# Optimization experiments

Measured on AMD Instinct MI355X. Metric: run time of the kernel, lower is better.

The kernel has to match this reference:

```python
import jax, jax.numpy as jnp
import numpy as np

N, E, H, O = 50000, 640000, 128, 2
N_LAYERS = 3


def setup_inputs() -> dict:
    key = jax.random.key(0)
    ks = jax.random.split(key, 20)
    s = 0.05
    inp = {
        "x": jax.random.normal(ks[0], (N, H), dtype=jnp.float32),
        "edge_index": jax.random.randint(ks[1], (2, E), 0, N, dtype=jnp.int64),
        "edge_type": jax.random.randint(ks[2], (E,), 0, 2, dtype=jnp.int64),
        # msg_sf MLP: Linear(2H->H), ReLU, Linear(H->H)
        "w1_sf": jax.random.normal(ks[3], (2 * H, H), jnp.float32) * s,
        "b1_sf": jnp.zeros((H,), jnp.float32),
        "w2_sf": jax.random.normal(ks[4], (H, H), jnp.float32) * s,
        "b2_sf": jnp.zeros((H,), jnp.float32),
        # msg_fd MLP
        "w1_fd": jax.random.normal(ks[5], (2 * H, H), jnp.float32) * s,
        "b1_fd": jnp.zeros((H,), jnp.float32),
        "w2_fd": jax.random.normal(ks[6], (H, H), jnp.float32) * s,
        "b2_fd": jnp.zeros((H,), jnp.float32),
        # GRUCell gru_h (PyTorch layout: [3H, in] / [3H, H], gate order r,z,n)
        "gru_w_ih": jax.random.normal(ks[7], (3 * H, H), jnp.float32) * s,
        "gru_w_hh": jax.random.normal(ks[8], (3 * H, H), jnp.float32) * s,
        "gru_b_ih": jnp.zeros((3 * H,), jnp.float32),
        "gru_b_hh": jnp.zeros((3 * H,), jnp.float32),
        # readout: Linear(H->H), ReLU, Linear(H->O)
        "wr1": jax.random.normal(ks[9], (H, H), jnp.float32) * s,
        "br1": jnp.zeros((H,), jnp.float32),
        "wr2": jax.random.normal(ks[10], (H, O), jnp.float32) * s,
        "br2": jnp.zeros((O,), jnp.float32),
    }
    return inp


def _mlp(ef, w1, b1, w2, b2):
    return jax.nn.relu(ef @ w1 + b1) @ w2 + b2


def _gru_cell(m, h, w_ih, w_hh, b_ih, b_hh):
    gi = m @ w_ih.T + b_ih  # [N, 3H]
    gh = h @ w_hh.T + b_hh  # [N, 3H]
    r = jax.nn.sigmoid(gi[:, :H] + gh[:, :H])
    z = jax.nn.sigmoid(gi[:, H:2 * H] + gh[:, H:2 * H])
    n = jnp.tanh(gi[:, 2 * H:] + r * gh[:, 2 * H:])
    return (1.0 - z) * n + z * h


def reference(x, edge_index, edge_type,
              w1_sf, b1_sf, w2_sf, b2_sf,
              w1_fd, b1_fd, w2_fd, b2_fd,
              gru_w_ih, gru_w_hh, gru_b_ih, gru_b_hh,
              wr1, br1, wr2, br2):
    src, tgt = edge_index[0], edge_index[1]
    is_sf = (edge_type == 0)[:, None]  # [E, 1]
    h = x
    for _ in range(N_LAYERS):
        # gather source/target node states and concatenate -> [E, 2H]
        ef = jnp.concatenate([h[src], h[tgt]], axis=-1)
        # per-edge message from the edge-type-specific MLP
        m = jnp.where(is_sf,
                      _mlp(ef, w1_sf, b1_sf, w2_sf, b2_sf),
                      _mlp(ef, w1_fd, b1_fd, w2_fd, b2_fd))
        # scatter-add into target nodes
        messages = jax.ops.segment_sum(m, tgt, num_segments=h.shape[0])
        # GRU node update (original's messages.mean(dim=1) is shape-invalid
        # for GRUCell; the runnable interpretation feeds messages directly)
        h = _gru_cell(messages, h, gru_w_ih, gru_w_hh, gru_b_ih, gru_b_hh)
    out = jax.nn.relu(h @ wr1 + br1) @ wr2 + br2
    return jax.nn.softmax(out, axis=1)
```

## Files before the change

### kernel.cpp

```cpp
#include <hip/hip_runtime.h>
#include <hip/hip_bf16.h>


#define NN 50000
#define EE 640000
#define HH 128
#define NBINS (2 * NN)
#define NBLKS 384

typedef __attribute__((ext_vector_type(8))) short short8;
typedef __attribute__((ext_vector_type(4))) float f32x4;

__device__ __forceinline__ unsigned short f2b(float f) {
  __hip_bfloat16 b = __float2bfloat16(f);
  return *reinterpret_cast<unsigned short*>(&b);
}
__device__ __forceinline__ float b2f_lo(unsigned int u) {
  union { unsigned int u; float f; } a; a.u = u << 16; return a.f;
}
__device__ __forceinline__ float b2f_hi(unsigned int u) {
  union { unsigned int u; float f; } a; a.u = u & 0xFFFF0000u; return a.f;
}

__device__ __forceinline__ void gload_lds16(const void* g, void* l) {
  __builtin_amdgcn_global_load_lds((const __attribute__((address_space(1))) void*)g,
                                   (__attribute__((address_space(3))) void*)l, 16, 0, 0);
}

__global__ __launch_bounds__(256) void k_init(const float* __restrict__ x, float* __restrict__ h,
                                              unsigned short* __restrict__ hbf) {
  int i = blockIdx.x * 256 + threadIdx.x;
  float v = x[i];
  h[i] = v;
  hbf[i] = f2b(v);
}

__global__ __launch_bounds__(256) void k_pack(
    const float* __restrict__ w1s, const float* __restrict__ w2s,
    const float* __restrict__ w1f, const float* __restrict__ w2f,
    const float* __restrict__ gwih, const float* __restrict__ gwhh,
    const float* __restrict__ gbih, const float* __restrict__ gbhh,
    unsigned short* __restrict__ pw1s, unsigned short* __restrict__ pw2s,
    unsigned short* __restrict__ pw1f, unsigned short* __restrict__ pw2f,
    unsigned short* __restrict__ pgru, float* __restrict__ bgr) {
  int i = blockIdx.x * 256 + threadIdx.x;
  if (i < 65536) {
    int ty = i >> 15, idx = i & 32767;
    int j = idx & 7, l = (idx >> 3) & 63, kn = idx >> 9;
    int ks = kn & 7, nt = kn >> 3;
    int k = ks * 32 + (l >> 4) * 8 + j, c = nt * 16 + (l & 15);
    const float* w = ty ? w1f : w1s;
    (ty ? pw1f : pw1s)[idx] = f2b(w[k * 128 + c]);
  } else if (i < 98304) {
    int i2 = i - 65536;
    int ty = i2 >> 14, idx = i2 & 16383;
    int j = idx & 7, l = (idx >> 3) & 63, kn = idx >> 9;
    int ks = kn & 3, nt = kn >> 2;
    int k = ks * 32 + (l >> 4) * 8 + j, c = nt * 16 + (l & 15);
    const float* w = ty ? w2f : w2s;
    (ty ? pw2f : pw2s)[idx] = f2b(w[k * 128 + c]);
  } else if (i < 98304 + 131072) {
    int idx = i - 98304;
    int j = idx & 7, l = (idx >> 3) & 63, kc = idx >> 9;
    int ks = kc & 7, ct = kc >> 3;
    int k = ks * 32 + (l >> 4) * 8 + j, c = ct * 16 + (l & 15);
    float v;
    if (c < 256)      v = (k < 128) ? gwih[c * 128 + k] : gwhh[c * 128 + (k - 128)];
    else if (c < 384) v = (k < 128) ? gwih[c * 128 + k] : 0.f;
    else              v = (k >= 128) ? gwhh[(c - 128) * 128 + (k - 128)] : 0.f;
    pgru[idx] = f2b(v);
  } else if (i < 98304 + 131072 + 512) {
    int j = i - (98304 + 131072);
    float v;
    if (j < 256)      v = gbih[j] + gbhh[j];
    else if (j < 384) v = gbih[j];
    else              v = gbhh[j - 128];
    bgr[j] = v;
  }
}

__global__ __launch_bounds__(256) void k_hist(const int* __restrict__ ei, const int* __restrict__ et,
                                              int* __restrict__ hist) {
  int e = blockIdx.x * 256 + threadIdx.x;
  int g = ei[EE + e];
  int ty = et[e];
  atomicAdd(&hist[ty * NN + g], 1);
}

__global__ __launch_bounds__(1024) void k_scan1(const int* __restrict__ hist, int* __restrict__ base,
                                                int* __restrict__ bsum) {
  __shared__ int sh[1024];
  int t = threadIdx.x;
  int i = blockIdx.x * 1024 + t;
  int v = (i < NBINS) ? hist[i] : 0;
  sh[t] = v;
  __syncthreads();
  for (int o = 1; o < 1024; o <<= 1) {
    int xv = (t >= o) ? sh[t - o] : 0;
    __syncthreads();
    sh[t] += xv;
    __syncthreads();
  }
  if (i < NBINS) base[i] = sh[t] - v;
  if (t == 1023) bsum[blockIdx.x] = sh[t];
}

__global__ __launch_bounds__(128) void k_scan2(int* __restrict__ bsum) {
  __shared__ int sh[128];
  int t = threadIdx.x;
  int v = (t < 98) ? bsum[t] : 0;
  sh[t] = v;
  __syncthreads();
  for (int o = 1; o < 128; o <<= 1) {
    int xv = (t >= o) ? sh[t - o] : 0;
    __syncthreads();
    sh[t] += xv;
    __syncthreads();
  }
  if (t < 98) bsum[t] = sh[t] - v;
}

__global__ __launch_bounds__(1024) void k_scan3(const int* __restrict__ bsum, int* __restrict__ base,
                                                int* __restrict__ cnt) {
  int i = blockIdx.x * 1024 + threadIdx.x;
  if (i < NBINS) {
    int b = base[i] + bsum[blockIdx.x];
    base[i] = b;
    if (i == NN) cnt[0] = b;
  }
}

__global__ __launch_bounds__(256) void k_scatter(const int* __restrict__ ei, const int* __restrict__ et,
                                                 int* __restrict__ woff, int* __restrict__ ssrc,
                                                 int* __restrict__ stgt) {
  int e = blockIdx.x * 256 + threadIdx.x;
  int s = ei[e], g = ei[EE + e], ty = et[e];
  int pos = atomicAdd(&woff[ty * NN + g], 1);
  ssrc[pos] = s;
  stgt[pos] = g;
}

__global__ __launch_bounds__(256, 2) void k_edge(
    const unsigned short* __restrict__ hbf,
    const int* __restrict__ ssrc, const int* __restrict__ stgt,
    const unsigned short* __restrict__ pw1s, const unsigned short* __restrict__ pw2s,
    const unsigned short* __restrict__ pw1f, const unsigned short* __restrict__ pw2f,
    const float* __restrict__ b1s, const float* __restrict__ b2s,
    const float* __restrict__ b1f, const float* __restrict__ b2f,
    float* __restrict__ msg, const int* __restrict__ cnt) {
  __shared__ char efA[16384];
  __shared__ char efB[16384];
  __shared__ char mC[17408];
  __shared__ int idxbuf[2][2][64];
  const int tid = threadIdx.x, l = tid & 63, w = tid >> 6;
  const int c0 = cnt[0];
  const int type = (blockIdx.x >= NBLKS) ? 1 : 0;
  const int bsub = type ? (blockIdx.x - NBLKS) : blockIdx.x;
  const int lo = type ? c0 : 0;
  const int hi = type ? EE : c0;
  const int ntile = (hi - lo + 63) >> 6;
  if (bsub >= ntile) return;
  const int nblk = 1 + (ntile - 1 - bsub) / NBLKS;
  const unsigned short* pw1 = type ? pw1f : pw1s;
  const unsigned short* pw2 = type ? pw2f : pw2s;
  const float* b1 = type ? b1f : b1s;
  const float* b2 = type ? b2f : b2s;

  short8 wb1[2][8];
#pragma unroll
  for (int q = 0; q < 2; q++) {
    int nt = 2 * w + q;
#pragma unroll
    for (int ks = 0; ks < 8; ks++)
      wb1[q][ks] = *(const short8*)(pw1 + ((nt * 8 + ks) * 64 + l) * 8);
  }
  float b1v[2], b2v[2];
  b1v[0] = b1[(2 * w) * 16 + (l & 15)];
  b1v[1] = b1[(2 * w + 1) * 16 + (l & 15)];
  b2v[0] = b2[(2 * w) * 16 + (l & 15)];
  b2v[1] = b2[(2 * w + 1) * 16 + (l & 15)];

  auto issue_gathers = [&](int slot) {
#pragma unroll
    for (int i = 0; i < 4; i++) {
      int r = w * 16 + i * 4 + (l >> 4);
      int j = (l & 15) ^ (r & 7);
      int nodeS = idxbuf[slot][0][r];
      gload_lds16(hbf + (size_t)nodeS * HH + j * 8, efA + w * 4096 + i * 1024);
      int nodeT = idxbuf[slot][1][r];
      if (nodeT < 0) nodeT = 0;
      gload_lds16(hbf + (size_t)nodeT * HH + j * 8, efB + w * 4096 + i * 1024);
    }
  };

  {
    int p0 = lo + bsub * 64 + (tid & 63);
    if (tid < 64) {
      int v = (p0 < hi) ? ssrc[p0] : 0;
      if (v < 0) v = 0;
      idxbuf[0][0][tid] = v;
    } else if (tid < 128) {
      int v = (p0 < hi) ? stgt[p0] : -1;
      idxbuf[0][1][tid & 63] = v;
    }
  }
  int ridx = (tid < 64) ? 0 : -1;
  {
    int p1 = lo + (bsub + NBLKS) * 64 + (tid & 63);
    if (tid < 128 && p1 < hi) ridx = (tid < 64) ? ssrc[p1] : stgt[p1];
  }
  asm volatile("s_waitcnt lgkmcnt(0)" ::: "memory");
  __builtin_amdgcn_s_barrier();
  issue_gathers(0);

  f32x4 zero4 = {0.f, 0.f, 0.f, 0.f};
  for (int k = 0; k < nblk; k++) {
    const int cur = k & 1, nxt = cur ^ 1;
    asm volatile("s_waitcnt vmcnt(0)" ::: "memory");
    __builtin_amdgcn_sched_barrier(0);
    __builtin_amdgcn_s_barrier();

    f32x4 acc[4][2];
#pragma unroll
    for (int mt = 0; mt < 4; mt++)
#pragma unroll
      for (int q = 0; q < 2; q++) acc[mt][q] = zero4;
    __builtin_amdgcn_s_setprio(1);
#pragma unroll
    for (int ks = 0; ks < 8; ks++) {
      const char* ef = (ks < 4) ? efA : efB;
      int ko = (ks & 3) * 64;
      short8 a[4];
#pragma unroll
      for (int mt = 0; mt < 4; mt++) {
        int row = mt * 16 + (l & 15);
        a[mt] = *(const short8*)(ef + row * 256 + ((ko + (l >> 4) * 16) ^ ((row & 7) << 4)));
      }
#pragma unroll
      for (int mt = 0; mt < 4; mt++)
#pragma unroll
        for (int q = 0; q < 2; q++)
          acc[mt][q] = __builtin_amdgcn_mfma_f32_16x16x32_bf16(a[mt], wb1[q][ks], acc[mt][q], 0, 0, 0);
    }
    __builtin_amdgcn_s_setprio(0);
    if (tid < 128) {
      int v = ridx;
      if (tid < 64 && v < 0) v = 0;
      idxbuf[nxt][tid >= 64 ? 1 : 0][tid & 63] = v;
    }
    {
      int p2 = lo + (bsub + (k + 2) * NBLKS) * 64 + (tid & 63);
      ridx = (tid < 64) ? 0 : -1;
      if (tid < 128 && p2 < hi) ridx = (tid < 64) ? ssrc[p2] : stgt[p2];
    }
#pragma unroll
    for (int mt = 0; mt < 4; mt++)
#pragma unroll
      for (int q = 0; q < 2; q++) {
        int col = (2 * w + q) * 16 + (l & 15);
#pragma unroll
        for (int r = 0; r < 4; r++) {
          int row = mt * 16 + (l >> 4) * 4 + r;
          float v = acc[mt][q][r] + b1v[q];
          v = v > 0.f ? v : 0.f;
          *(unsigned short*)(mC + row * 256 + ((col * 2) ^ ((row & 7) << 4))) = f2b(v);
        }
      }
    asm volatile("s_waitcnt lgkmcnt(0)" ::: "memory");
    __builtin_amdgcn_s_barrier();

    short8 wb2[2][4];
#pragma unroll
    for (int q = 0; q < 2; q++)
#pragma unroll
      for (int ks = 0; ks < 4; ks++)
        wb2[q][ks] = *(const short8*)(pw2 + (((2 * w + q) * 4 + ks) * 64 + l) * 8);
    if (k + 1 < nblk) issue_gathers(nxt);
#pragma unroll
    for (int mt = 0; mt < 4; mt++)
#pragma unroll
      for (int q = 0; q < 2; q++) acc[mt][q] = zero4;
    __builtin_amdgcn_s_setprio(1);
#pragma unroll
    for (int ks = 0; ks < 4; ks++) {
      short8 a[4];
#pragma unroll
      for (int mt = 0; mt < 4; mt++) {
        int row = mt * 16 + (l & 15);
        a[mt] = *(const short8*)(mC + row * 256 + ((ks * 64 + (l >> 4) * 16) ^ ((row & 7) << 4)));
      }
#pragma unroll
      for (int mt = 0; mt < 4; mt++)
#pragma unroll
        for (int q = 0; q < 2; q++)
          acc[mt][q] = __builtin_amdgcn_mfma_f32_16x16x32_bf16(a[mt], wb2[q][ks], acc[mt][q], 0, 0, 0);
    }
    __builtin_amdgcn_s_setprio(0);
    __builtin_amdgcn_s_barrier();

#pragma unroll
    for (int mt = 0; mt < 4; mt++)
#pragma unroll
      for (int q = 0; q < 2; q++) {
        int col = (2 * w + q) * 16 + (l & 15);
        int e0 = mt * 16 + (l >> 4) * 4;
        f32x4 v = acc[mt][q];
        unsigned int u0 = (unsigned int)f2b(v.x + b2v[q]) | ((unsigned int)f2b(v.y + b2v[q]) << 16);
        unsigned int u1 = (unsigned int)f2b(v.z + b2v[q]) | ((unsigned int)f2b(v.w + b2v[q]) << 16);
        *(unsigned int*)(mC + col * 132 + e0 * 2) = u0;
        *(unsigned int*)(mC + col * 132 + e0 * 2 + 4) = u1;
      }
    asm volatile("s_waitcnt lgkmcnt(0)" ::: "memory");
    __builtin_amdgcn_s_barrier();

    {
      int f = tid & 127, grp = tid >> 7;
      float accum = 0.f;
      int curg = idxbuf[cur][1][grp * 32];
#pragma unroll
      for (int jj = 0; jj < 8; jj++) {
        int4 tg = *(const int4*)&idxbuf[cur][1][grp * 32 + jj * 4];
        unsigned int m0 = *(const unsigned int*)(mC + f * 132 + (grp * 32 + jj * 4) * 2);
        unsigned int m1 = *(const unsigned int*)(mC + f * 132 + (grp * 32 + jj * 4) * 2 + 4);
        float vv[4];
        vv[0] = b2f_lo(m0); vv[1] = b2f_hi(m0);
        vv[2] = b2f_lo(m1); vv[3] = b2f_hi(m1);
        int gg[4] = {tg.x, tg.y, tg.z, tg.w};
#pragma unroll
        for (int r = 0; r < 4; r++) {
          if (gg[r] != curg) {
            if (curg >= 0) atomicAdd(&msg[(size_t)curg * HH + f], accum);
            accum = 0.f;
            curg = gg[r];
          }
          accum += vv[r];
        }
      }
      if (curg >= 0) atomicAdd(&msg[(size_t)curg * HH + f], accum);
    }
  }
}

__global__ __launch_bounds__(256) void k_gru(
    const float* __restrict__ msg, const unsigned short* __restrict__ pgru,
    const float* __restrict__ bgr, float* __restrict__ h, unsigned short* __restrict__ hbf) {
  __shared__ char amh[64 * 512];
  int tid = threadIdx.x, l = tid & 63, w = tid >> 6;
  int n0 = blockIdx.x * 64;
#pragma unroll
  for (int i = 0; i < 8; i++) {
    int c = tid + i * 256;
    int r = c >> 5, cc = c & 31;
    int node = n0 + r; if (node > NN - 1) node = NN - 1;
    float4 v = *((const float4*)(msg + (size_t)node * HH) + cc);
    uint2 u;
    u.x = (unsigned int)f2b(v.x) | ((unsigned int)f2b(v.y) << 16);
    u.y = (unsigned int)f2b(v.z) | ((unsigned int)f2b(v.w) << 16);
    *(uint2*)(amh + r * 512 + ((cc * 8) ^ ((r & 7) << 4))) = u;
  }
#pragma unroll
  for (int i = 0; i < 4; i++) {
    int c = tid + i * 256;
    int r = c >> 4, cc = c & 15;
    int node = n0 + r; if (node > NN - 1) node = NN - 1;
    int4 v = *((const int4*)(hbf + (size_t)node * HH) + cc);
    *(int4*)(amh + r * 512 + ((256 + cc * 16) ^ ((r & 7) << 4))) = v;
  }
  __syncthreads();

  f32x4 zero4 = {0.f, 0.f, 0.f, 0.f};
  f32x4 acc[4][8];
#pragma unroll
  for (int mt = 0; mt < 4; mt++)
#pragma unroll
    for (int t = 0; t < 8; t++) acc[mt][t] = zero4;
#pragma unroll
  for (int ks = 0; ks < 8; ks++) {
    short8 a[4];
#pragma unroll
    for (int mt = 0; mt < 4; mt++) {
      int row = mt * 16 + (l & 15);
      a[mt] = *(const short8*)(amh + row * 512 + ((ks * 64 + (l >> 4) * 16) ^ ((row & 7) << 4)));
    }
#pragma unroll
    for (int t = 0; t < 8; t++) {
      int ct = w + 4 * t;
      short8 bf = *(const short8*)(pgru + ((ct * 8 + ks) * 64 + l) * 8);
#pragma unroll
      for (int mt = 0; mt < 4; mt++)
        acc[mt][t] = __builtin_amdgcn_mfma_f32_16x16x32_bf16(a[mt], bf, acc[mt][t], 0, 0, 0);
    }
  }

#pragma unroll
  for (int tt = 0; tt < 2; tt++) {
    int ct = w + 4 * tt;
    int j = ct * 16 + (l & 15);
    float br = bgr[j], bz = bgr[128 + j], bgi = bgr[256 + j], bgh = bgr[384 + j];
#pragma unroll
    for (int mt = 0; mt < 4; mt++) {
#pragma unroll
      for (int r = 0; r < 4; r++) {
        int row = mt * 16 + (l >> 4) * 4 + r;
        int node = n0 + row;
        if (node < NN) {
          float hold = h[(size_t)node * HH + j];
          float ur = acc[mt][tt][r] + br;
          float uz = acc[mt][tt + 2][r] + bz;
          float gi = acc[mt][tt + 4][r] + bgi;
          float gh = acc[mt][tt + 6][r] + bgh;
          float rr = 1.f / (1.f + __expf(-ur));
          float zz = 1.f / (1.f + __expf(-uz));
          float xx = gi + rr * gh;
          xx = fminf(fmaxf(xx, -15.f), 15.f);
          float ex = __expf(2.f * xx);
          float nn2 = (ex - 1.f) / (ex + 1.f);
          float hn = (1.f - zz) * nn2 + zz * hold;
          h[(size_t)node * HH + j] = hn;
          hbf[(size_t)node * HH + j] = f2b(hn);
        }
      }
    }
  }
}

__global__ __launch_bounds__(256) void k_read(const float* __restrict__ h,
                                              const float* __restrict__ wr1, const float* __restrict__ br1,
                                              const float* __restrict__ wr2, const float* __restrict__ br2,
                                              float* __restrict__ out) {
  __shared__ float sh[16][128];
  int tid = threadIdx.x, l = tid & 63, w = tid >> 6;
  int nb = blockIdx.x * 16;
#pragma unroll
  for (int i = 0; i < 8; i++) {
    int c = tid + i * 256;
    int r = c >> 7, k = c & 127;
    int node = nb + r; if (node > NN - 1) node = NN - 1;
    sh[r][k] = h[(size_t)node * HH + k];
  }
  __syncthreads();
  float a1[4] = {0.f, 0.f, 0.f, 0.f}, a2[4] = {0.f, 0.f, 0.f, 0.f};
  for (int k = 0; k < 128; k++) {
    float w1a = wr1[k * 128 + l];
    float w1b = wr1[k * 128 + l + 64];
#pragma unroll
    for (int n = 0; n < 4; n++) {
      float hv = sh[w * 4 + n][k];
      a1[n] += hv * w1a;
      a2[n] += hv * w1b;
    }
  }
  float bra = br1[l], brb = br1[l + 64];
  float w20 = wr2[l * 2 + 0], w21 = wr2[l * 2 + 1];
  float w20b = wr2[(l + 64) * 2 + 0], w21b = wr2[(l + 64) * 2 + 1];
#pragma unroll
  for (int n = 0; n < 4; n++) {
    float h1 = fmaxf(a1[n] + bra, 0.f), h2 = fmaxf(a2[n] + brb, 0.f);
    float l0 = h1 * w20 + h2 * w20b;
    float l1 = h1 * w21 + h2 * w21b;
#pragma unroll
    for (int o = 32; o > 0; o >>= 1) {
      l0 += __shfl_xor(l0, o);
      l1 += __shfl_xor(l1, o);
    }
    if (l == 0) {
      int node = nb + w * 4 + n;
      if (node < NN) {
        l0 += br2[0];
        l1 += br2[1];
        float mx = fmaxf(l0, l1);
        float e0 = __expf(l0 - mx), e1 = __expf(l1 - mx);
        float s = e0 + e1;
        out[node * 2 + 0] = e0 / s;
        out[node * 2 + 1] = e1 / s;
      }
    }
  }
}

extern "C" void kernel_launch(void* const* d_in, const int* in_sizes, int n_in,
                              void* d_out, int out_size, void* d_ws, size_t ws_size,
                              hipStream_t stream) {
  const float* x    = (const float*)d_in[0];
  const int*   ei   = (const int*)d_in[1];
  const int*   et   = (const int*)d_in[2];
  const float* w1s  = (const float*)d_in[3];
  const float* b1s  = (const float*)d_in[4];
  const float* w2s  = (const float*)d_in[5];
  const float* b2s  = (const float*)d_in[6];
  const float* w1f  = (const float*)d_in[7];
  const float* b1f  = (const float*)d_in[8];
  const float* w2f  = (const float*)d_in[9];
  const float* b2f  = (const float*)d_in[10];
  const float* gwih = (const float*)d_in[11];
  const float* gwhh = (const float*)d_in[12];
  const float* gbih = (const float*)d_in[13];
  const float* gbhh = (const float*)d_in[14];
  const float* wr1  = (const float*)d_in[15];
  const float* br1  = (const float*)d_in[16];
  const float* wr2  = (const float*)d_in[17];
  const float* br2  = (const float*)d_in[18];
  float* out = (float*)d_out;
  (void)in_sizes; (void)n_in; (void)out_size; (void)ws_size;

  char* p = (char*)d_ws;
  size_t off = 0;
  auto alloc = [&](size_t sz) {
    char* r = p + off;
    off = (off + sz + 255) & ~(size_t)255;
    return r;
  };
  float* h             = (float*)alloc((size_t)NN * HH * 4);
  unsigned short* hbf  = (unsigned short*)alloc((size_t)NN * HH * 2);
  float* msg           = (float*)alloc((size_t)NN * HH * 4);
  int* ssrc            = (int*)alloc((size_t)EE * 4);
  int* stgt            = (int*)alloc((size_t)EE * 4);
  int* hist            = (int*)alloc((size_t)NBINS * 4);
  int* base            = (int*)alloc((size_t)NBINS * 4);
  int* woff            = (int*)alloc((size_t)NBINS * 4);
  int* bsum            = (int*)alloc(128 * 4);
  int* cnt             = (int*)alloc(16);
  unsigned short* pw1s = (unsigned short*)alloc(32768 * 2);
  unsigned short* pw2s = (unsigned short*)alloc(16384 * 2);
  unsigned short* pw1f = (unsigned short*)alloc(32768 * 2);
  unsigned short* pw2f = (unsigned short*)alloc(16384 * 2);
  unsigned short* pgru = (unsigned short*)alloc(131072 * 2);
  float* bgr           = (float*)alloc(512 * 4);

  hipMemsetAsync(hist, 0, (size_t)NBINS * 4, stream);
  k_init<<<NN * HH / 256, 256, 0, stream>>>(x, h, hbf);
  k_pack<<<898, 256, 0, stream>>>(w1s, w2s, w1f, w2f, gwih, gwhh, gbih, gbhh,
                                  pw1s, pw2s, pw1f, pw2f, pgru, bgr);
  k_hist<<<EE / 256, 256, 0, stream>>>(ei, et, hist);
  k_scan1<<<98, 1024, 0, stream>>>(hist, base, bsum);
  k_scan2<<<1, 128, 0, stream>>>(bsum);
  k_scan3<<<98, 1024, 0, stream>>>(bsum, base, cnt);
  hipMemcpyAsync(woff, base, (size_t)NBINS * 4, hipMemcpyDeviceToDevice, stream);
  k_scatter<<<EE / 256, 256, 0, stream>>>(ei, et, woff, ssrc, stgt);

  for (int layer = 0; layer < 3; layer++) {
    hipMemsetAsync(msg, 0, (size_t)NN * HH * 4, stream);
    k_edge<<<2 * NBLKS, 256, 0, stream>>>(hbf, ssrc, stgt, pw1s, pw2s, pw1f, pw2f,
                                          b1s, b2s, b1f, b2f, msg, cnt);
    k_gru<<<(NN + 63) / 64, 256, 0, stream>>>(msg, pgru, bgr, h, hbf);
  }
  k_read<<<NN / 16, 256, 0, stream>>>(h, wr1, br1, wr2, br2, out);
}
```

Before: 687.1 us.

## Fuse message-buffer zeroing into GRU kernel and shrink edge kernel LDS

Replaces the per-layer memset of the 25.6 MB message accumulator with zero stores issued by the GRU kernel right after it reads each row, keeping only one up-front memset. In the edge kernel, index buffers become 16-bit and the transposed message tile uses an XOR-swizzled 128-byte row layout instead of 132-byte padding, with 8-byte LDS accesses, reducing LDS footprint and instruction count. The 16-bit indices assume node ids fit in 16 bits, but N is 50000 so ids fit only as unsigned values and 0xFFFF is reserved as a sentinel. Zeroing inside the GRU adds write traffic there but removes a separate full-buffer pass.

```diff
diff --git a/kernel.cpp b/kernel.cpp
--- a/kernel.cpp
+++ b/kernel.cpp
@@ -150,8 +150,8 @@
     float* __restrict__ msg, const int* __restrict__ cnt) {
   __shared__ char efA[16384];
   __shared__ char efB[16384];
-  __shared__ char mC[17408];
-  __shared__ int idxbuf[2][2][64];
+  __shared__ char mC[16384];
+  __shared__ unsigned short idxbuf[2][2][64];
   const int tid = threadIdx.x, l = tid & 63, w = tid >> 6;
   const int c0 = cnt[0];
   const int type = (blockIdx.x >= NBLKS) ? 1 : 0;
@@ -188,7 +188,7 @@
       int nodeS = idxbuf[slot][0][r];
       gload_lds16(hbf + (size_t)nodeS * HH + j * 8, efA + w * 4096 + i * 1024);
       int nodeT = idxbuf[slot][1][r];
-      if (nodeT < 0) nodeT = 0;
+      if (nodeT == 0xFFFF) nodeT = 0;
       gload_lds16(hbf + (size_t)nodeT * HH + j * 8, efB + w * 4096 + i * 1024);
     }
   };
@@ -198,10 +198,10 @@
     if (tid < 64) {
       int v = (p0 < hi) ? ssrc[p0] : 0;
       if (v < 0) v = 0;
-      idxbuf[0][0][tid] = v;
+      idxbuf[0][0][tid] = (unsigned short)v;
     } else if (tid < 128) {
       int v = (p0 < hi) ? stgt[p0] : -1;
-      idxbuf[0][1][tid & 63] = v;
+      idxbuf[0][1][tid & 63] = (unsigned short)v;
     }
   }
   int ridx = (tid < 64) ? 0 : -1;
@@ -246,7 +246,7 @@
     if (tid < 128) {
       int v = ridx;
       if (tid < 64 && v < 0) v = 0;
-      idxbuf[nxt][tid >= 64 ? 1 : 0][tid & 63] = v;
+      idxbuf[nxt][tid >= 64 ? 1 : 0][tid & 63] = (unsigned short)v;
     }
     {
       int p2 = lo + (bsub + (k + 2) * NBLKS) * 64 + (tid & 63);
@@ -305,10 +305,10 @@
         int col = (2 * w + q) * 16 + (l & 15);
         int e0 = mt * 16 + (l >> 4) * 4;
         f32x4 v = acc[mt][q];
-        unsigned int u0 = (unsigned int)f2b(v.x + b2v[q]) | ((unsigned int)f2b(v.y + b2v[q]) << 16);
-        unsigned int u1 = (unsigned int)f2b(v.z + b2v[q]) | ((unsigned int)f2b(v.w + b2v[q]) << 16);
-        *(unsigned int*)(mC + col * 132 + e0 * 2) = u0;
-        *(unsigned int*)(mC + col * 132 + e0 * 2 + 4) = u1;
+        uint2 uu;
+        uu.x = (unsigned int)f2b(v.x + b2v[q]) | ((unsigned int)f2b(v.y + b2v[q]) << 16);
+        uu.y = (unsigned int)f2b(v.z + b2v[q]) | ((unsigned int)f2b(v.w + b2v[q]) << 16);
+        *(uint2*)(mC + col * 128 + ((e0 * 2) ^ ((col & 7) << 4))) = uu;
       }
     asm volatile("s_waitcnt lgkmcnt(0)" ::: "memory");
     __builtin_amdgcn_s_barrier();
@@ -319,40 +319,44 @@
       int curg = idxbuf[cur][1][grp * 32];
 #pragma unroll
       for (int jj = 0; jj < 8; jj++) {
-        int4 tg = *(const int4*)&idxbuf[cur][1][grp * 32 + jj * 4];
-        unsigned int m0 = *(const unsigned int*)(mC + f * 132 + (grp * 32 + jj * 4) * 2);
-        unsigned int m1 = *(const unsigned int*)(mC + f * 132 + (grp * 32 + jj * 4) * 2 + 4);
+        int eb = grp * 32 + jj * 4;
+        ushort4 tg = *(const ushort4*)&idxbuf[cur][1][eb];
+        uint2 mv = *(const uint2*)(mC + f * 128 + ((eb * 2) ^ ((f & 7) << 4)));
         float vv[4];
-        vv[0] = b2f_lo(m0); vv[1] = b2f_hi(m0);
-        vv[2] = b2f_lo(m1); vv[3] = b2f_hi(m1);
+        vv[0] = b2f_lo(mv.x); vv[1] = b2f_hi(mv.x);
+        vv[2] = b2f_lo(mv.y); vv[3] = b2f_hi(mv.y);
         int gg[4] = {tg.x, tg.y, tg.z, tg.w};
 #pragma unroll
         for (int r = 0; r < 4; r++) {
           if (gg[r] != curg) {
-            if (curg >= 0) atomicAdd(&msg[(size_t)curg * HH + f], accum);
+            if (curg != 0xFFFF) atomicAdd(&msg[(size_t)curg * HH + f], accum);
             accum = 0.f;
             curg = gg[r];
           }
           accum += vv[r];
         }
       }
-      if (curg >= 0) atomicAdd(&msg[(size_t)curg * HH + f], accum);
+      if (curg != 0xFFFF) atomicAdd(&msg[(size_t)curg * HH + f], accum);
     }
   }
 }
 
 __global__ __launch_bounds__(256) void k_gru(
     const float* __restrict__ msg, const unsigned short* __restrict__ pgru,
-    const float* __restrict__ bgr, float* __restrict__ h, unsigned short* __restrict__ hbf) {
+    const float* __restrict__ bgr, float* __restrict__ h, unsigned short* __restrict__ hbf,
+    float* __restrict__ msgw, int dz) {
   __shared__ char amh[64 * 512];
   int tid = threadIdx.x, l = tid & 63, w = tid >> 6;
   int n0 = blockIdx.x * 64;
+  f32x4 zero4 = {0.f, 0.f, 0.f, 0.f};
 #pragma unroll
   for (int i = 0; i < 8; i++) {
     int c = tid + i * 256;
     int r = c >> 5, cc = c & 31;
-    int node = n0 + r; if (node > NN - 1) node = NN - 1;
+    int node0 = n0 + r;
+    int node = node0 > NN - 1 ? NN - 1 : node0;
     float4 v = *((const float4*)(msg + (size_t)node * HH) + cc);
+    if (dz && node0 < NN) *((f32x4*)(msgw + (size_t)node0 * HH) + cc) = zero4;
     uint2 u;
     u.x = (unsigned int)f2b(v.x) | ((unsigned int)f2b(v.y) << 16);
     u.y = (unsigned int)f2b(v.z) | ((unsigned int)f2b(v.w) << 16);
@@ -368,7 +372,6 @@
   }
   __syncthreads();
 
-  f32x4 zero4 = {0.f, 0.f, 0.f, 0.f};
   f32x4 acc[4][8];
 #pragma unroll
   for (int mt = 0; mt < 4; mt++)
@@ -537,12 +540,12 @@
   k_scan3<<<98, 1024, 0, stream>>>(bsum, base, cnt);
   hipMemcpyAsync(woff, base, (size_t)NBINS * 4, hipMemcpyDeviceToDevice, stream);
   k_scatter<<<EE / 256, 256, 0, stream>>>(ei, et, woff, ssrc, stgt);
+  hipMemsetAsync(msg, 0, (size_t)NN * HH * 4, stream);
 
   for (int layer = 0; layer < 3; layer++) {
-    hipMemsetAsync(msg, 0, (size_t)NN * HH * 4, stream);
     k_edge<<<2 * NBLKS, 256, 0, stream>>>(hbf, ssrc, stgt, pw1s, pw2s, pw1f, pw2f,
                                           b1s, b2s, b1f, b2f, msg, cnt);
-    k_gru<<<(NN + 63) / 64, 256, 0, stream>>>(msg, pgru, bgr, h, hbf);
+    k_gru<<<(NN + 63) / 64, 256, 0, stream>>>(msg, pgru, bgr, h, hbf, msg, layer < 2 ? 1 : 0);
   }
   k_read<<<NN / 16, 256, 0, stream>>>(h, wr1, br1, wr2, br2, out);
 }
```

Measured after the change: 671.4 us. -2.3%, faster.
